# Optimization experiments

Hardware: AMD Instinct MI355X
Metric: run time of the kernel (lower is better)

The kernel has to match this reference:

```python
import jax, jax.numpy as jnp
import numpy as np

N = 500_000   # total nodes across all graphs in the batch
B = 8192      # number of graphs
D = 128       # node_hidden_size
G = 2 * D     # graph_hidden_size = 2 * node_hidden_size (DGMG GraphEmbed)


def setup_inputs() -> dict:
    key = jax.random.key(0)
    ks = jax.random.split(key, 8)
    hv = jax.random.normal(ks[0], (N, D), dtype=jnp.float32)
    # sorted segment ids: node -> graph index (ragged batch, flat layout)
    seg_ids = jnp.sort(jax.random.randint(ks[1], (N,), 0, B, dtype=jnp.int32))
    # index of the latest node of each graph in the flat node array
    last_idx = jax.random.randint(ks[2], (B,), 0, N, dtype=jnp.int32)
    # AddEdge action per graph (0 = no edge, 1 = add edge)
    a = jax.random.randint(ks[3], (B,), 0, 2, dtype=jnp.int32)
    # GraphEmbed params: gate Linear(D->1), projection Linear(D->G)
    Wg = jax.random.normal(ks[4], (D, 1), dtype=jnp.float32) * 0.05
    bg = jnp.zeros((1,), dtype=jnp.float32)
    Wp = jax.random.normal(ks[5], (D, G), dtype=jnp.float32) * 0.05
    bp = jnp.zeros((G,), dtype=jnp.float32)
    # AddEdge decision head: Linear(G + D -> 1)
    We = jax.random.normal(ks[6], (G + D, 1), dtype=jnp.float32) * 0.05
    be = jnp.zeros((1,), dtype=jnp.float32)
    return {"hv": hv, "Wg": Wg, "bg": bg, "Wp": Wp, "bp": bp,
            "We": We, "be": be, "seg_ids": seg_ids,
            "last_idx": last_idx, "a": a}


def reference(hv, Wg, bg, Wp, bp, We, be, seg_ids, last_idx, a):
    # GraphEmbed: gated sum of projected node embeddings per graph
    gate = jax.nn.sigmoid(hv @ Wg + bg)                       # [N, 1]
    proj = hv @ Wp + bp                                       # [N, G]
    graph_embed = jax.ops.segment_sum(gate * proj, seg_ids,
                                      num_segments=B)         # [B, G]
    # latest node embedding per graph (batch_src_embed)
    src_embed = hv[last_idx]                                  # [B, D]
    # AddEdge logit (dropout is identity in eval)
    feat = jnp.concatenate([graph_embed, src_embed], axis=1)  # [B, G+D]
    logit = feat @ We + be                                    # [B, 1]
    # bernoulli_action_log_prob: [logsigmoid(-logit), logsigmoid(logit)]
    log_probs = jnp.concatenate([jax.nn.log_sigmoid(-logit),
                                 jax.nn.log_sigmoid(logit)], axis=1)  # [B, 2]
    sample_log_prob = jnp.take_along_axis(log_probs, a[:, None].astype(jnp.int32), axis=1)  # [B, 1]
    return sample_log_prob
```

## Files before the change

### kernel.cpp

```cpp
#include <hip/hip_runtime.h>
#include <math.h>

#define D 128
#define G 256


__global__ void prep_kernel(const float* __restrict__ Wp,
                            const float* __restrict__ bp,
                            const float* __restrict__ We,
                            float* __restrict__ u,
                            float* __restrict__ c,
                            float* __restrict__ s,
                            int B) {
    int b  = blockIdx.x;
    int li = threadIdx.x;

    if (b >= 129) {
        int idx4 = (b - 129) * 64 + li;
        if (idx4 * 4 + 3 < B) ((float4*)s)[idx4] = make_float4(0.f, 0.f, 0.f, 0.f);
        else {
            for (int j = idx4 * 4; j < B; ++j) s[j] = 0.f;
        }
        return;
    }

    const float* row = (b < D) ? (Wp + (size_t)b * G) : bp;
    float4 rv = ((const float4*)row)[li];
    float4 wv = ((const float4*)We)[li];
    float p = rv.x * wv.x + rv.y * wv.y + rv.z * wv.z + rv.w * wv.w;
    #pragma unroll
    for (int m = 32; m >= 1; m >>= 1) p += __shfl_xor(p, m, 64);
    if (li == 0) {
        if (b < D) u[b] = p;
        else       *c  = p;
    }
}

__global__ void node_kernel(const float* __restrict__ hv,
                            const float* __restrict__ Wg,
                            const float* __restrict__ bg,
                            const int*   __restrict__ seg_ids,
                            const float* __restrict__ u,
                            const float* __restrict__ cptr,
                            float*       __restrict__ s,
                            int N, int chunk) {
    int tid  = blockIdx.x * blockDim.x + threadIdx.x;
    int wave = tid >> 6;
    int lane = threadIdx.x & 63;
    int half = lane >> 5;
    int li   = lane & 31;

    int start = wave * chunk;
    if (start >= N) return;
    int end = min(start + chunk, N);

    const float4* hv4 = (const float4*)hv;
    float4 wg4 = ((const float4*)Wg)[li];
    float4 u4  = ((const float4*)u)[li];
    float  bgv = *bg;
    float  cv  = *cptr;

    int   cur = -1;
    float acc = 0.f;

    for (int r0 = start; r0 < end; r0 += 2) {
        int row = r0 + half;
        float val = 0.f;
        int   seg = -1;
        if (row < end) {
            float4 v = hv4[(size_t)row * 32 + li];
            float p1 = v.x * wg4.x + v.y * wg4.y + v.z * wg4.z + v.w * wg4.w;
            float p2 = v.x * u4.x  + v.y * u4.y  + v.z * u4.z  + v.w * u4.w;
            #pragma unroll
            for (int m = 16; m >= 1; m >>= 1) {
                p1 += __shfl_xor(p1, m, 64);
                p2 += __shfl_xor(p2, m, 64);
            }
            float gate = 1.f / (1.f + __expf(-(p1 + bgv)));
            val = gate * (p2 + cv);
            seg = seg_ids[row];
        }
        if (li == 0 && seg >= 0) {
            if (seg != cur) {
                if (cur >= 0) atomicAdd(&s[cur], acc);
                cur = seg;
                acc = val;
            } else {
                acc += val;
            }
        }
    }
    if (li == 0 && cur >= 0) atomicAdd(&s[cur], acc);
}

__global__ void graph_kernel(const float* __restrict__ hv,
                             const float* __restrict__ We,
                             const float* __restrict__ be,
                             const int*   __restrict__ last_idx,
                             const int*   __restrict__ a,
                             const float* __restrict__ s,
                             float*       __restrict__ out,
                             int B) {
    int tid = blockIdx.x * blockDim.x + threadIdx.x;
    int g   = tid >> 5;
    int li  = threadIdx.x & 31;
    if (g >= B) return;

    int row = last_idx[g];
    float4 v = ((const float4*)hv)[(size_t)row * 32 + li];
    float4 w = ((const float4*)We)[64 + li];
    float p = v.x * w.x + v.y * w.y + v.z * w.z + v.w * w.w;
    #pragma unroll
    for (int m = 16; m >= 1; m >>= 1) p += __shfl_xor(p, m, 64);

    if (li == 0) {
        float logit = s[g] + p + *be;
        float x = (a[g] != 0) ? logit : -logit;
        out[g] = fminf(x, 0.f) - log1pf(__expf(-fabsf(x)));
    }
}

extern "C" void kernel_launch(void* const* d_in, const int* in_sizes, int n_in,
                              void* d_out, int out_size, void* d_ws, size_t ws_size,
                              hipStream_t stream) {
    const float* hv       = (const float*)d_in[0];
    const float* Wg       = (const float*)d_in[1];
    const float* bg       = (const float*)d_in[2];
    const float* Wp       = (const float*)d_in[3];
    const float* bp       = (const float*)d_in[4];
    const float* We       = (const float*)d_in[5];
    const float* be       = (const float*)d_in[6];
    const int*   seg_ids  = (const int*)d_in[7];
    const int*   last_idx = (const int*)d_in[8];
    const int*   a        = (const int*)d_in[9];
    float*       out      = (float*)d_out;

    int N = in_sizes[0] / D;
    int B = in_sizes[8];

    float* u = (float*)d_ws;
    float* c = (float*)((char*)d_ws + 512);
    float* s = (float*)((char*)d_ws + 1024);

    int nzero = (B / 4 + 63) / 64;
    prep_kernel<<<129 + nzero, 64, 0, stream>>>(Wp, bp, We, u, c, s, B);

    const int nblocks = 2048;
    int waves = nblocks * 256 / 64;
    int chunk = (N + waves - 1) / waves;
    chunk = (chunk + 1) & ~1;
    node_kernel<<<nblocks, 256, 0, stream>>>(hv, Wg, bg, seg_ids, u, c, s, N, chunk);

    int gblocks = (B + 7) / 8;
    graph_kernel<<<gblocks, 256, 0, stream>>>(hv, We, be, last_idx, a, s, out, B);
}
```

Before: 52.57 us.

## Compute per-node src-embed dot in node kernel, shrink final kernel to scalar gather

The node kernel now also computes each node's dot product with the src part of We and writes it to a per-node scalar buffer. The final kernel then gathers one float per graph instead of re-reading a 512-byte hv row and doing a warp reduction. This removes a random gather of 8192 hv rows in exchange for an extra shuffle reduction per node and a 2 MB scalar write in the streaming kernel.

```diff
diff --git a/kernel.cpp b/kernel.cpp
--- a/kernel.cpp
+++ b/kernel.cpp
@@ -42,7 +42,9 @@
                             const int*   __restrict__ seg_ids,
                             const float* __restrict__ u,
                             const float* __restrict__ cptr,
+                            const float* __restrict__ We,
                             float*       __restrict__ s,
+                            float*       __restrict__ pv,
                             int N, int chunk) {
     int tid  = blockIdx.x * blockDim.x + threadIdx.x;
     int wave = tid >> 6;
@@ -57,6 +59,7 @@
     const float4* hv4 = (const float4*)hv;
     float4 wg4 = ((const float4*)Wg)[li];
     float4 u4  = ((const float4*)u)[li];
+    float4 w24 = ((const float4*)We)[64 + li];
     float  bgv = *bg;
     float  cv  = *cptr;
 
@@ -71,14 +74,17 @@
             float4 v = hv4[(size_t)row * 32 + li];
             float p1 = v.x * wg4.x + v.y * wg4.y + v.z * wg4.z + v.w * wg4.w;
             float p2 = v.x * u4.x  + v.y * u4.y  + v.z * u4.z  + v.w * u4.w;
+            float p3 = v.x * w24.x + v.y * w24.y + v.z * w24.z + v.w * w24.w;
             #pragma unroll
             for (int m = 16; m >= 1; m >>= 1) {
                 p1 += __shfl_xor(p1, m, 64);
                 p2 += __shfl_xor(p2, m, 64);
+                p3 += __shfl_xor(p3, m, 64);
             }
             float gate = 1.f / (1.f + __expf(-(p1 + bgv)));
             val = gate * (p2 + cv);
             seg = seg_ids[row];
+            if (li == 0) pv[row] = p3;
         }
         if (li == 0 && seg >= 0) {
             if (seg != cur) {
@@ -93,31 +99,18 @@
     if (li == 0 && cur >= 0) atomicAdd(&s[cur], acc);
 }
 
-__global__ void graph_kernel(const float* __restrict__ hv,
-                             const float* __restrict__ We,
+__global__ void final_kernel(const float* __restrict__ s,
+                             const float* __restrict__ pv,
                              const float* __restrict__ be,
                              const int*   __restrict__ last_idx,
                              const int*   __restrict__ a,
-                             const float* __restrict__ s,
                              float*       __restrict__ out,
                              int B) {
-    int tid = blockIdx.x * blockDim.x + threadIdx.x;
-    int g   = tid >> 5;
-    int li  = threadIdx.x & 31;
+    int g = blockIdx.x * blockDim.x + threadIdx.x;
     if (g >= B) return;
-
-    int row = last_idx[g];
-    float4 v = ((const float4*)hv)[(size_t)row * 32 + li];
-    float4 w = ((const float4*)We)[64 + li];
-    float p = v.x * w.x + v.y * w.y + v.z * w.z + v.w * w.w;
-    #pragma unroll
-    for (int m = 16; m >= 1; m >>= 1) p += __shfl_xor(p, m, 64);
-
-    if (li == 0) {
-        float logit = s[g] + p + *be;
-        float x = (a[g] != 0) ? logit : -logit;
-        out[g] = fminf(x, 0.f) - log1pf(__expf(-fabsf(x)));
-    }
+    float logit = s[g] + pv[last_idx[g]] + *be;
+    float x = (a[g] != 0) ? logit : -logit;
+    out[g] = fminf(x, 0.f) - log1pf(__expf(-fabsf(x)));
 }
 
 extern "C" void kernel_launch(void* const* d_in, const int* in_sizes, int n_in,
@@ -138,9 +131,10 @@
     int N = in_sizes[0] / D;
     int B = in_sizes[8];
 
-    float* u = (float*)d_ws;
-    float* c = (float*)((char*)d_ws + 512);
-    float* s = (float*)((char*)d_ws + 1024);
+    float* u  = (float*)d_ws;
+    float* c  = (float*)((char*)d_ws + 512);
+    float* s  = (float*)((char*)d_ws + 1024);
+    float* pv = (float*)((char*)d_ws + 65536);
 
     int nzero = (B / 4 + 63) / 64;
     prep_kernel<<<129 + nzero, 64, 0, stream>>>(Wp, bp, We, u, c, s, B);
@@ -149,8 +143,8 @@
     int waves = nblocks * 256 / 64;
     int chunk = (N + waves - 1) / waves;
     chunk = (chunk + 1) & ~1;
-    node_kernel<<<nblocks, 256, 0, stream>>>(hv, Wg, bg, seg_ids, u, c, s, N, chunk);
+    node_kernel<<<nblocks, 256, 0, stream>>>(hv, Wg, bg, seg_ids, u, c, We, s, pv, N, chunk);
 
-    int gblocks = (B + 7) / 8;
-    graph_kernel<<<gblocks, 256, 0, stream>>>(hv, We, be, last_idx, a, s, out, B);
+    int fblocks = (B + 255) / 256;
+    final_kernel<<<fblocks, 256, 0, stream>>>(s, pv, be, last_idx, a, out, B);
 }
```

After: 63.90 us. 21.6% more time.
